# Optimization experiments

Measured on AMD Instinct MI355X. Metric: run time of the kernel, lower is better.

The kernel has to match this reference:

```python
import jax, jax.numpy as jnp
import numpy as np

N_NODES = 100000
N_EDGES = 1600000
NEG_SLOPE = 0.2  # DGL GATConv default leaky_relu slope
BN_EPS = 1e-5


def setup_inputs() -> dict:
    key = jax.random.key(0)
    ks = jax.random.split(key, 10)
    feats = jax.random.normal(ks[0], (N_NODES, 128), dtype=jnp.float32)
    src = jax.random.randint(ks[1], (N_EDGES,), 0, N_NODES, dtype=jnp.int64)
    dst = jax.random.randint(ks[2], (N_EDGES,), 0, N_NODES, dtype=jnp.int64)
    fc_w = jax.random.normal(ks[3], (256, 128), dtype=jnp.float32) * 0.05   # H*D x in_feats
    attn_l = jax.random.normal(ks[4], (4, 64), dtype=jnp.float32) * 0.05
    attn_r = jax.random.normal(ks[5], (4, 64), dtype=jnp.float32) * 0.05
    res_w = jax.random.normal(ks[6], (256, 128), dtype=jnp.float32) * 0.05  # residual projection
    bias = jax.random.normal(ks[7], (4, 64), dtype=jnp.float32) * 0.05
    gamma = jnp.ones((64,), dtype=jnp.float32)
    beta = jnp.zeros((64,), dtype=jnp.float32)
    return {"feats": feats, "src": src, "dst": dst, "fc_w": fc_w,
            "attn_l": attn_l, "attn_r": attn_r, "res_w": res_w,
            "bias": bias, "gamma": gamma, "beta": beta}


def reference(feats, src, dst, fc_w, attn_l, attn_r, res_w, bias, gamma, beta):
    N = feats.shape[0]
    H, D = attn_l.shape
    # projected features [N, H, D] (feat_drop is identity in eval mode)
    h = (feats @ fc_w.T).reshape(N, H, D)
    # per-node attention logits [N, H]
    el = jnp.sum(h * attn_l[None], axis=-1)
    er = jnp.sum(h * attn_r[None], axis=-1)
    # edge logits, leaky relu
    e = el[src] + er[dst]                       # [E, H]
    e = jnp.where(e > 0, e, NEG_SLOPE * e)
    # numerically stable segment softmax over incoming edges of each dst node
    m = jax.ops.segment_max(e, dst, num_segments=N)       # [N, H]
    ex = jnp.exp(e - m[dst])                               # [E, H]
    s = jax.ops.segment_sum(ex, dst, num_segments=N)       # [N, H]
    alpha = ex / s[dst]                                    # [E, H]
    # weighted message aggregation: scatter-add alpha * h_src into dst
    msg = h[src] * alpha[:, :, None]                       # [E, H, D]
    rst = jax.ops.segment_sum(msg, dst, num_segments=N)    # [N, H, D]
    # residual projection + bias + activation (elu)
    res = (feats @ res_w.T).reshape(N, H, D)
    rst = jax.nn.elu(rst + res + bias[None])
    # mean over heads -> [N, D]
    out = rst.mean(axis=1)
    # BatchNorm1d (training stats: biased variance over the node/batch axis)
    mu = out.mean(axis=0)
    var = out.var(axis=0)
    return (out - mu) * jax.lax.rsqrt(var + BN_EPS) * gamma + beta
```

## Files before the change

kernel.cpp:

```cpp
#include <hip/hip_runtime.h>

#define N_NODES 100000
#define N_EDGES 1600000
#define NEG_SLOPE 0.2f
#define BN_EPS 1e-5f

typedef __attribute__((ext_vector_type(8))) short short8;
typedef __attribute__((ext_vector_type(4))) float floatx4;
typedef __attribute__((ext_vector_type(8))) unsigned short u16x8;

static const size_t OFF_AB   = 0;
static const size_t OFF_BB   = 25624576;
static const size_t OFF_H    = 25755648;
static const size_t OFF_RES  = 76956672;
static const size_t OFF_EL   = 128156672;
static const size_t OFF_ER   = 129757184;
static const size_t OFF_DEG  = 131357184;
static const size_t OFF_RS   = 131757184;
static const size_t OFF_BNP  = 132157568;
static const size_t OFF_ESRC = 132557568;
static const size_t OFF_BS   = 142157568;

__device__ __forceinline__ unsigned short f2bf(float x) {
  unsigned int u = __float_as_uint(x);
  unsigned int r = (u + 0x7fffu + ((u >> 16) & 1u)) >> 16;
  return (unsigned short)r;
}
__device__ __forceinline__ float bf2f(unsigned short u) {
  return __uint_as_float(((unsigned int)u) << 16);
}

__global__ __launch_bounds__(256) void k_pre(
    const float* __restrict__ feats, const float* __restrict__ fc_w,
    const float* __restrict__ res_w, const int* __restrict__ dst,
    unsigned short* __restrict__ Ab, unsigned short* __restrict__ Bb,
    int* __restrict__ deg, unsigned short* __restrict__ hbuf,
    float* __restrict__ el, int* __restrict__ rank)
{
  const int b = blockIdx.x;
  if (b < 6256) {
    int c = b * 256 + threadIdx.x;
    int r = c >> 4, j = c & 15;
    unsigned short v[8];
    if (r < N_NODES) {
      const float* p = feats + (size_t)r * 128 + j * 8;
      float4 a = *(const float4*)p, bb = *(const float4*)(p + 4);
      v[0]=f2bf(a.x); v[1]=f2bf(a.y); v[2]=f2bf(a.z); v[3]=f2bf(a.w);
      v[4]=f2bf(bb.x); v[5]=f2bf(bb.y); v[6]=f2bf(bb.z); v[7]=f2bf(bb.w);
    } else {
      for (int i = 0; i < 8; i++) v[i] = 0;
    }
    size_t idx = (size_t)(r >> 7) * 2048 + ((r >> 4) & 7) * 256 + (j >> 2) * 64
               + (r & 15) + 16 * (j & 3);
    *(short8*)(Ab + idx * 8) = *(short8*)v;
  } else if (b < 12506) {
    int e = (b - 6256) * 256 + threadIdx.x;
    if (e < N_EDGES) rank[e] = atomicAdd(&deg[dst[e]], 1);
  } else if (b < 12538) {
    int c = (b - 12506) * 256 + threadIdx.x;
    int n = c >> 4, j = c & 15;
    const float* W = (n < 256) ? (fc_w + (size_t)n * 128) : (res_w + (size_t)(n - 256) * 128);
    const float* p = W + j * 8;
    float4 a = *(const float4*)p, bb = *(const float4*)(p + 4);
    unsigned short v[8];
    v[0]=f2bf(a.x); v[1]=f2bf(a.y); v[2]=f2bf(a.z); v[3]=f2bf(a.w);
    v[4]=f2bf(bb.x); v[5]=f2bf(bb.y); v[6]=f2bf(bb.z); v[7]=f2bf(bb.w);
    size_t idx = (size_t)(n >> 7) * 2048 + ((n >> 4) & 7) * 256 + (j >> 2) * 64
               + (n & 15) + 16 * (j & 3);
    *(short8*)(Bb + idx * 8) = *(short8*)v;
  } else {
    const int t = threadIdx.x;
    hbuf[(size_t)N_NODES * 256 + t] = 0;
    if (t < 4) el[N_NODES * 4 + t] = -1e30f;
  }
}

__global__ __launch_bounds__(256) void k_scan1(const int* __restrict__ deg,
                                               int* __restrict__ rs, int* __restrict__ bsums)
{
  __shared__ int tmp[256];
  const int t = threadIdx.x;
  const int base = blockIdx.x * 1024 + t * 4;
  int v0 = 0, v1 = 0, v2 = 0, v3 = 0;
  if (base + 0 < N_NODES) v0 = (deg[base + 0] + 3) & ~3;
  if (base + 1 < N_NODES) v1 = (deg[base + 1] + 3) & ~3;
  if (base + 2 < N_NODES) v2 = (deg[base + 2] + 3) & ~3;
  if (base + 3 < N_NODES) v3 = (deg[base + 3] + 3) & ~3;
  const int tsum = v0 + v1 + v2 + v3;
  tmp[t] = tsum;
  __syncthreads();
  for (int o = 1; o < 256; o <<= 1) {
    int x = (t >= o) ? tmp[t - o] : 0;
    __syncthreads();
    tmp[t] += x;
    __syncthreads();
  }
  const int excl = tmp[t] - tsum;
  if (base + 0 < N_NODES) rs[base + 0] = excl;
  if (base + 1 < N_NODES) rs[base + 1] = excl + v0;
  if (base + 2 < N_NODES) rs[base + 2] = excl + v0 + v1;
  if (base + 3 < N_NODES) rs[base + 3] = excl + v0 + v1 + v2;
  if (t == 255) bsums[blockIdx.x] = tmp[t];
}

__global__ __launch_bounds__(256) void k_scan3(int* __restrict__ rs,
                                               const int* __restrict__ bsums,
                                               const int* __restrict__ deg,
                                               int* __restrict__ esrc)
{
  __shared__ int sb[128];
  const int t = threadIdx.x;
  int raw = 0;
  if (t < 128) { raw = (t < 98) ? bsums[t] : 0; sb[t] = raw; }
  __syncthreads();
  for (int o = 1; o < 128; o <<= 1) {
    int x = (t >= o && t < 128) ? sb[t - o] : 0;
    __syncthreads();
    if (t < 128) sb[t] += x;
    __syncthreads();
  }
  if (t < 128) sb[t] -= raw;
  __syncthreads();
  const int i = blockIdx.x * 256 + t;
  if (i < N_NODES) {
    int v = rs[i] + sb[i >> 10];
    rs[i] = v;
    const int d = deg[i];
    const int pd = (d + 3) & ~3;
    for (int j = d; j < pd; j++) esrc[v + j] = N_NODES;
    if (i == N_NODES - 1) rs[N_NODES] = v + pd;
  }
}

__global__ __launch_bounds__(256) void k_place(const int* __restrict__ src,
                                               const int* __restrict__ dst,
                                               const int* __restrict__ rs,
                                               const int* __restrict__ rank,
                                               int* __restrict__ esrc)
{
  int e = blockIdx.x * 256 + threadIdx.x;
  if (e >= N_EDGES) return;
  esrc[rs[dst[e]] + rank[e]] = src[e];
}

__global__ __launch_bounds__(256) void k_mm(
    const unsigned short* __restrict__ Ab, const unsigned short* __restrict__ Bb,
    const float* __restrict__ bias, const float* __restrict__ attn_l,
    const float* __restrict__ attn_r,
    unsigned short* __restrict__ hbuf, unsigned short* __restrict__ resbuf,
    float* __restrict__ el, float* __restrict__ er)
{
  __shared__ unsigned short sA[16384];
  const int tid = threadIdx.x;
  const int w = tid >> 6, L = tid & 63;
  const int blk = blockIdx.x;

  {
    const unsigned short* ga = Ab + (size_t)blk * 16384;
    #pragma unroll
    for (int i = 0; i < 8; i++) {
      int off = (i * 256 + w * 64) * 8;
      __builtin_amdgcn_global_load_lds(
          (const __attribute__((address_space(1))) unsigned int*)(ga + off + L * 8),
          (__attribute__((address_space(3))) unsigned int*)(sA + off),
          16, 0, 0);
    }
  }
  const int mh = w & 1, nh = w >> 1;
  __syncthreads();

  for (int wb = 0; wb < 2; ++wb) {
    const int nb = blockIdx.y + wb * 2;
    floatx4 acc[4][4] = {};
    const unsigned short* gb = Bb + ((size_t)nb * 2048 + nh * 4 * 256) * 8 + L * 8;
    #pragma unroll
    for (int s = 0; s < 4; s++) {
      short8 a[4], b[4];
      #pragma unroll
      for (int t = 0; t < 4; t++)
        a[t] = *(const short8*)(sA + ((mh * 4 + t) * 256 + s * 64 + L) * 8);
      #pragma unroll
      for (int t = 0; t < 4; t++)
        b[t] = *(const short8*)(gb + ((size_t)t * 256 + s * 64) * 8);
      #pragma unroll
      for (int mt = 0; mt < 4; mt++)
        #pragma unroll
        for (int nt = 0; nt < 4; nt++)
          acc[mt][nt] = __builtin_amdgcn_mfma_f32_16x16x32_bf16(a[mt], b[nt], acc[mt][nt], 0, 0, 0);
    }

    const int q = L >> 4, cn = L & 15;
    const int r0 = blk * 128 + mh * 64;
    if (nb < 2) {
      const int head = nb * 2 + nh;
      const int col0 = nb * 128 + nh * 64;
      float al[4], ar[4];
      #pragma unroll
      for (int nt = 0; nt < 4; nt++) {
        al[nt] = attn_l[head * 64 + nt * 16 + cn];
        ar[nt] = attn_r[head * 64 + nt * 16 + cn];
      }
      #pragma unroll
      for (int mt = 0; mt < 4; mt++)
        #pragma unroll
        for (int r = 0; r < 4; r++) {
          const int row = r0 + mt * 16 + q * 4 + r;
          float pl = 0.f, pr = 0.f;
          #pragma unroll
          for (int nt = 0; nt < 4; nt++) {
            pl = fmaf(acc[mt][nt][r], al[nt], pl);
            pr = fmaf(acc[mt][nt][r], ar[nt], pr);
          }
          #pragma unroll
          for (int o = 1; o < 16; o <<= 1) {
            pl += __shfl_xor(pl, o, 64);
            pr += __shfl_xor(pr, o, 64);
          }
          if (row < N_NODES) {
            #pragma unroll
            for (int nt = 0; nt < 4; nt++)
              hbuf[(size_t)row * 256 + col0 + nt * 16 + cn] = f2bf(acc[mt][nt][r]);
            if (cn == 0) {
              el[row * 4 + head] = pl;
              er[row * 4 + head] = pr;
            }
          }
        }
    } else {
      const int rc0 = (nb - 2) * 128 + nh * 64;
      #pragma unroll
      for (int mt = 0; mt < 4; mt++)
        #pragma unroll
        for (int r = 0; r < 4; r++) {
          const int row = r0 + mt * 16 + q * 4 + r;
          if (row < N_NODES)
            #pragma unroll
            for (int nt = 0; nt < 4; nt++) {
              float v = acc[mt][nt][r] + bias[rc0 + nt * 16 + cn];
              resbuf[(size_t)row * 256 + rc0 + nt * 16 + cn] = f2bf(v);
            }
        }
    }
  }
}

#define RFL(x) __builtin_amdgcn_readfirstlane(x)

#define GATHER(X) do { \
  const int s_ = (lane & 32) ? sn##X.y : sn##X.x; \
  hv##X = *(const u16x8*)(hbuf + (size_t)s_ * 256 + li8); \
  ev##X = el[s_ * 4 + head]; \
} while (0)

#define PRO(X, B) do { \
  if ((B) < p_end) { sn##X = *(const int2*)(esrc + (B)); GATHER(X); } \
} while (0)

#define COMPUTE(X) do { \
  float e_ = ev##X + ern; \
  e_ = fmaxf(e_, NEG_SLOPE * e_); \
  const float w_ = __expf(e_); \
  ssum += w_; \
  accA.x = fmaf(w_, bf2f(hv##X[0]), accA.x); \
  accA.y = fmaf(w_, bf2f(hv##X[1]), accA.y); \
  accA.z = fmaf(w_, bf2f(hv##X[2]), accA.z); \
  accA.w = fmaf(w_, bf2f(hv##X[3]), accA.w); \
  accB.x = fmaf(w_, bf2f(hv##X[4]), accB.x); \
  accB.y = fmaf(w_, bf2f(hv##X[5]), accB.y); \
  accB.z = fmaf(w_, bf2f(hv##X[6]), accB.z); \
  accB.w = fmaf(w_, bf2f(hv##X[7]), accB.w); \
} while (0)

#define FIN(ND) do { \
  float st_ = ssum + __shfl_xor(ssum, 32, 64); \
  float a0_ = accA.x + __shfl_xor(accA.x, 32, 64); \
  float a1_ = accA.y + __shfl_xor(accA.y, 32, 64); \
  float a2_ = accA.z + __shfl_xor(accA.z, 32, 64); \
  float a3_ = accA.w + __shfl_xor(accA.w, 32, 64); \
  float a4_ = accB.x + __shfl_xor(accB.x, 32, 64); \
  float a5_ = accB.y + __shfl_xor(accB.y, 32, 64); \
  float a6_ = accB.z + __shfl_xor(accB.z, 32, 64); \
  float a7_ = accB.w + __shfl_xor(accB.w, 32, 64); \
  const float inv_ = (st_ > 0.f) ? (1.0f / st_) : 0.f; \
  a0_ = fmaf(a0_, inv_, bf2f(rv_cur[0])); \
  a1_ = fmaf(a1_, inv_, bf2f(rv_cur[1])); \
  a2_ = fmaf(a2_, inv_, bf2f(rv_cur[2])); \
  a3_ = fmaf(a3_, inv_, bf2f(rv_cur[3])); \
  a4_ = fmaf(a4_, inv_, bf2f(rv_cur[4])); \
  a5_ = fmaf(a5_, inv_, bf2f(rv_cur[5])); \
  a6_ = fmaf(a6_, inv_, bf2f(rv_cur[6])); \
  a7_ = fmaf(a7_, inv_, bf2f(rv_cur[7])); \
  a0_ = (a0_ > 0.f) ? a0_ : (__expf(a0_) - 1.f); \
  a1_ = (a1_ > 0.f) ? a1_ : (__expf(a1_) - 1.f); \
  a2_ = (a2_ > 0.f) ? a2_ : (__expf(a2_) - 1.f); \
  a3_ = (a3_ > 0.f) ? a3_ : (__expf(a3_) - 1.f); \
  a4_ = (a4_ > 0.f) ? a4_ : (__expf(a4_) - 1.f); \
  a5_ = (a5_ > 0.f) ? a5_ : (__expf(a5_) - 1.f); \
  a6_ = (a6_ > 0.f) ? a6_ : (__expf(a6_) - 1.f); \
  a7_ = (a7_ > 0.f) ? a7_ : (__expf(a7_) - 1.f); \
  a0_ += __shfl_xor(a0_, 8, 64);  a0_ += __shfl_xor(a0_, 16, 64); \
  a1_ += __shfl_xor(a1_, 8, 64);  a1_ += __shfl_xor(a1_, 16, 64); \
  a2_ += __shfl_xor(a2_, 8, 64);  a2_ += __shfl_xor(a2_, 16, 64); \
  a3_ += __shfl_xor(a3_, 8, 64);  a3_ += __shfl_xor(a3_, 16, 64); \
  a4_ += __shfl_xor(a4_, 8, 64);  a4_ += __shfl_xor(a4_, 16, 64); \
  a5_ += __shfl_xor(a5_, 8, 64);  a5_ += __shfl_xor(a5_, 16, 64); \
  a6_ += __shfl_xor(a6_, 8, 64);  a6_ += __shfl_xor(a6_, 16, 64); \
  a7_ += __shfl_xor(a7_, 8, 64);  a7_ += __shfl_xor(a7_, 16, 64); \
  if (lane < 8) { \
    float4 o1_, o2_; \
    o1_.x = a0_ * 0.25f; o1_.y = a1_ * 0.25f; o1_.z = a2_ * 0.25f; o1_.w = a3_ * 0.25f; \
    o2_.x = a4_ * 0.25f; o2_.y = a5_ * 0.25f; o2_.z = a6_ * 0.25f; o2_.w = a7_ * 0.25f; \
    *(float4*)(out + (size_t)(ND) * 64 + li8) = o1_; \
    *(float4*)(out + (size_t)(ND) * 64 + li8 + 4) = o2_; \
    atomicAdd(&ls[li8 + 0], o1_.x); atomicAdd(&ls[li8 + 1], o1_.y); \
    atomicAdd(&ls[li8 + 2], o1_.z); atomicAdd(&ls[li8 + 3], o1_.w); \
    atomicAdd(&ls[li8 + 4], o2_.x); atomicAdd(&ls[li8 + 5], o2_.y); \
    atomicAdd(&ls[li8 + 6], o2_.z); atomicAdd(&ls[li8 + 7], o2_.w); \
    atomicAdd(&lq[li8 + 0], o1_.x * o1_.x); atomicAdd(&lq[li8 + 1], o1_.y * o1_.y); \
    atomicAdd(&lq[li8 + 2], o1_.z * o1_.z); atomicAdd(&lq[li8 + 3], o1_.w * o1_.w); \
    atomicAdd(&lq[li8 + 4], o2_.x * o2_.x); atomicAdd(&lq[li8 + 5], o2_.y * o2_.y); \
    atomicAdd(&lq[li8 + 6], o2_.z * o2_.z); atomicAdd(&lq[li8 + 7], o2_.w * o2_.w); \
  } \
} while (0)

#define BOUNDARY() \
  while (p == nend) { \
    FIN(nu); \
    accA.x=0.f; accA.y=0.f; accA.z=0.f; accA.w=0.f; \
    accB.x=0.f; accB.y=0.f; accB.z=0.f; accB.w=0.f; ssum = 0.f; \
    nu++; \
    nend = nendN; ern = ernN; rv_cur = rvN; \
    const int f1_ = (nu + 1 < N_NODES) ? (nu + 1) : (N_NODES - 1); \
    const int f2_ = (nu + 2 <= N_NODES) ? (nu + 2) : N_NODES; \
    nendN = RFL(rs[f2_]); \
    ernN = er[f1_ * 4 + head]; \
    rvN = *(const u16x8*)(resbuf + (size_t)f1_ * 256 + li8); \
  }

#define STEP(CUR, GAT) do { \
  if (p + 12 < p_end) GATHER(GAT); \
  if (p + 16 < p_end) sn##CUR = *(const int2*)(esrc + p + 16); \
  __builtin_amdgcn_sched_barrier(0); \
  BOUNDARY(); \
  COMPUTE(CUR); \
} while (0)

__global__ __launch_bounds__(256, 4) void k_agg(
    const unsigned short* __restrict__ hbuf, const unsigned short* __restrict__ resbuf,
    const float* __restrict__ el, const float* __restrict__ er,
    const int* __restrict__ rs, const int* __restrict__ esrc,
    float* __restrict__ out, float* __restrict__ bn)
{
  __shared__ float ls[64], lq[64];
  const int lane = threadIdx.x & 63;
  const int li = lane & 31;
  const int head = li >> 3;
  const int li8 = li * 8;
  const int wid = blockIdx.x * 4 + (threadIdx.x >> 6);
  const int nW = gridDim.x * 4;

  if (threadIdx.x < 64) { ls[threadIdx.x] = 0.f; lq[threadIdx.x] = 0.f; }
  __syncthreads();

  const int n0 = (int)(((long long)wid * N_NODES) / nW);
  const int n1 = (int)(((long long)(wid + 1) * N_NODES) / nW);

  if (n0 < n1) {
    int nu = RFL(n0);
    const int p_end = RFL(rs[n1]);
    int nend = RFL(rs[nu + 1]);
    int f1 = (nu + 1 < N_NODES) ? (nu + 1) : (N_NODES - 1);
    int f2 = (nu + 2 <= N_NODES) ? (nu + 2) : N_NODES;
    int nendN = RFL(rs[f2]);
    float ern  = er[nu * 4 + head];
    float ernN = er[f1 * 4 + head];
    u16x8 rv_cur = *(const u16x8*)(resbuf + (size_t)nu * 256 + li8);
    u16x8 rvN    = *(const u16x8*)(resbuf + (size_t)f1 * 256 + li8);

    float4 accA = make_float4(0.f, 0.f, 0.f, 0.f);
    float4 accB = make_float4(0.f, 0.f, 0.f, 0.f);
    float ssum = 0.f;

    int2 snA, snB, snC, snD, snE, snF, snG, snH;
    float evA, evB, evC, evD, evE, evF, evG, evH;
    u16x8 hvA, hvB, hvC, hvD, hvE, hvF, hvG, hvH;

    int p = RFL(rs[nu]);
    PRO(A, p);      PRO(B, p + 2);  PRO(C, p + 4);  PRO(D, p + 6);
    PRO(E, p + 8);  PRO(F, p + 10);
    if (p + 12 < p_end) snG = *(const int2*)(esrc + p + 12);
    if (p + 14 < p_end) snH = *(const int2*)(esrc + p + 14);
    __builtin_amdgcn_sched_barrier(0);

    while (p < p_end) {
      STEP(A, G); p += 2; if (p >= p_end) break;
      STEP(B, H); p += 2; if (p >= p_end) break;
      STEP(C, A); p += 2; if (p >= p_end) break;
      STEP(D, B); p += 2; if (p >= p_end) break;
      STEP(E, C); p += 2; if (p >= p_end) break;
      STEP(F, D); p += 2; if (p >= p_end) break;
      STEP(G, E); p += 2; if (p >= p_end) break;
      STEP(H, F); p += 2;
    }

    while (nu < n1) {
      FIN(nu);
      accA.x=0.f; accA.y=0.f; accA.z=0.f; accA.w=0.f;
      accB.x=0.f; accB.y=0.f; accB.z=0.f; accB.w=0.f; ssum = 0.f;
      nu++;
      if (nu < n1) rv_cur = *(const u16x8*)(resbuf + (size_t)nu * 256 + li8);
    }
  }

  __syncthreads();
  const int t = threadIdx.x;
  if (t < 64)       atomicAdd(&bn[t * 16], ls[t]);
  else if (t < 128) atomicAdd(&bn[t * 16], lq[t - 64]);
}

__global__ __launch_bounds__(256) void k_bn_apply(float* __restrict__ out,
                                                  const float* __restrict__ bn,
                                                  const float* __restrict__ gamma,
                                                  const float* __restrict__ beta)
{
  __shared__ float sc[64], sh[64];
  const int t = threadIdx.x;
  if (t < 64) {
    float mean = bn[t * 16] * (1.0f / N_NODES);
    float var = bn[(t + 64) * 16] * (1.0f / N_NODES) - mean * mean;
    float s = gamma[t] * rsqrtf(var + BN_EPS);
    sc[t] = s;
    sh[t] = beta[t] - mean * s;
  }
  __syncthreads();
  const int i = blockIdx.x * 256 + t;
  if (i >= N_NODES * 16) return;
  const int d0 = (i & 15) * 4;
  float4 v = *(float4*)(out + (size_t)i * 4);
  v.x = fmaf(v.x, sc[d0 + 0], sh[d0 + 0]);
  v.y = fmaf(v.y, sc[d0 + 1], sh[d0 + 1]);
  v.z = fmaf(v.z, sc[d0 + 2], sh[d0 + 2]);
  v.w = fmaf(v.w, sc[d0 + 3], sh[d0 + 3]);
  *(float4*)(out + (size_t)i * 4) = v;
}

extern "C" void kernel_launch(void* const* d_in, const int* in_sizes, int n_in,
                              void* d_out, int out_size, void* d_ws, size_t ws_size,
                              hipStream_t stream)
{
  const float* feats  = (const float*)d_in[0];
  const int*   src    = (const int*)d_in[1];
  const int*   dst    = (const int*)d_in[2];
  const float* fc_w   = (const float*)d_in[3];
  const float* attn_l = (const float*)d_in[4];
  const float* attn_r = (const float*)d_in[5];
  const float* res_w  = (const float*)d_in[6];
  const float* bias   = (const float*)d_in[7];
  const float* gamma  = (const float*)d_in[8];
  const float* beta   = (const float*)d_in[9];

  char* ws = (char*)d_ws;
  unsigned short* Ab     = (unsigned short*)(ws + OFF_AB);
  unsigned short* Bb     = (unsigned short*)(ws + OFF_BB);
  unsigned short* hbuf   = (unsigned short*)(ws + OFF_H);
  unsigned short* resbuf = (unsigned short*)(ws + OFF_RES);
  float* elb    = (float*)(ws + OFF_EL);
  float* erb    = (float*)(ws + OFF_ER);
  int*   deg    = (int*)(ws + OFF_DEG);
  int*   rsb    = (int*)(ws + OFF_RS);
  float* bnb    = (float*)(ws + OFF_BNP);
  int*   esrc   = (int*)(ws + OFF_ESRC);
  int*   bsums  = (int*)(ws + OFF_BS);
  float* outp   = (float*)d_out;
  int*   rankp  = (int*)d_out;

  hipMemsetAsync(deg, 0, N_NODES * sizeof(int), stream);
  hipMemsetAsync(bnb, 0, 128 * 16 * sizeof(float), stream);

  k_pre<<<12539, 256, 0, stream>>>(feats, fc_w, res_w, dst, Ab, Bb, deg, hbuf, elb, rankp);
  k_scan1<<<98, 256, 0, stream>>>(deg, rsb, bsums);
  k_scan3<<<391, 256, 0, stream>>>(rsb, bsums, deg, esrc);
  k_place<<<6250, 256, 0, stream>>>(src, dst, rsb, rankp, esrc);
  k_mm<<<dim3(782, 2), 256, 0, stream>>>(Ab, Bb, bias, attn_l, attn_r,
                                         hbuf, resbuf, elb, erb);
  k_agg<<<2048, 256, 0, stream>>>(hbuf, resbuf, elb, erb, rsb, esrc, outp, bnb);
  k_bn_apply<<<6250, 256, 0, stream>>>(outp, bnb, gamma, beta);
}
```

Baseline: 454.6 us.

## Precompute per-edge exp attention weights during CSR placement, drop bound checks in aggregation

Moves k_place after the matmul and has it compute each edge's leaky-relu and exp logit for all four heads, storing them as bf16 in CSR order in a buffer that reuses the Ab region. The aggregation kernel then loads one precomputed weight per edge instead of randomly gathering el[src] and computing exp. Padding slots and a 16-entry tail are zero-filled so the prefetch loop can drop its bounds checks. The trade is an extra scattered write of 8 bytes per edge, plus bf16 rounding of the attention weights, which may cost accuracy.

```diff
diff --git a/kernel.cpp b/kernel.cpp
--- a/kernel.cpp
+++ b/kernel.cpp
@@ -35,7 +35,7 @@
     const float* __restrict__ res_w, const int* __restrict__ dst,
     unsigned short* __restrict__ Ab, unsigned short* __restrict__ Bb,
     int* __restrict__ deg, unsigned short* __restrict__ hbuf,
-    float* __restrict__ el, int* __restrict__ rank)
+    int* __restrict__ rank)
 {
   const int b = blockIdx.x;
   if (b < 6256) {
@@ -69,9 +69,7 @@
                + (n & 15) + 16 * (j & 3);
     *(short8*)(Bb + idx * 8) = *(short8*)v;
   } else {
-    const int t = threadIdx.x;
-    hbuf[(size_t)N_NODES * 256 + t] = 0;
-    if (t < 4) el[N_NODES * 4 + t] = -1e30f;
+    hbuf[(size_t)N_NODES * 256 + threadIdx.x] = 0;
   }
 }
 
@@ -128,19 +126,11 @@
     const int d = deg[i];
     const int pd = (d + 3) & ~3;
     for (int j = d; j < pd; j++) esrc[v + j] = N_NODES;
-    if (i == N_NODES - 1) rs[N_NODES] = v + pd;
-  }
-}
-
-__global__ __launch_bounds__(256) void k_place(const int* __restrict__ src,
-                                               const int* __restrict__ dst,
-                                               const int* __restrict__ rs,
-                                               const int* __restrict__ rank,
-                                               int* __restrict__ esrc)
-{
-  int e = blockIdx.x * 256 + threadIdx.x;
-  if (e >= N_EDGES) return;
-  esrc[rs[dst[e]] + rank[e]] = src[e];
+    if (i == N_NODES - 1) {
+      rs[N_NODES] = v + pd;
+      for (int j = 0; j < 16; j++) esrc[v + pd + j] = N_NODES;
+    }
+  }
 }
 
 __global__ __launch_bounds__(256) void k_mm(
@@ -244,31 +234,60 @@
   }
 }
 
+__global__ __launch_bounds__(256) void k_place(
+    const int* __restrict__ src, const int* __restrict__ dst,
+    const int* __restrict__ rs, const int* __restrict__ rank,
+    const int* __restrict__ deg,
+    const float* __restrict__ el, const float* __restrict__ er,
+    int* __restrict__ esrc, unsigned short* __restrict__ wb)
+{
+  const int b = blockIdx.x;
+  if (b < 6250) {
+    const int e = b * 256 + threadIdx.x;
+    if (e >= N_EDGES) return;
+    const int d = dst[e], s = src[e];
+    const int pos = rs[d] + rank[e];
+    esrc[pos] = s;
+    const float4 l4 = *(const float4*)(el + (size_t)s * 4);
+    const float4 r4 = *(const float4*)(er + (size_t)d * 4);
+    float e0 = l4.x + r4.x; e0 = fmaxf(e0, NEG_SLOPE * e0);
+    float e1 = l4.y + r4.y; e1 = fmaxf(e1, NEG_SLOPE * e1);
+    float e2 = l4.z + r4.z; e2 = fmaxf(e2, NEG_SLOPE * e2);
+    float e3 = l4.w + r4.w; e3 = fmaxf(e3, NEG_SLOPE * e3);
+    ushort4 w4;
+    w4.x = f2bf(__expf(e0)); w4.y = f2bf(__expf(e1));
+    w4.z = f2bf(__expf(e2)); w4.w = f2bf(__expf(e3));
+    *(ushort4*)(wb + (size_t)pos * 4) = w4;
+  } else {
+    const int i = (b - 6250) * 256 + threadIdx.x;
+    if (i >= N_NODES) return;
+    const int d = deg[i], pd = (d + 3) & ~3;
+    const int v = rs[i];
+    const ushort4 z4 = make_ushort4(0, 0, 0, 0);
+    for (int j = d; j < pd; j++) *(ushort4*)(wb + (size_t)(v + j) * 4) = z4;
+    if (i == N_NODES - 1)
+      for (int j = 0; j < 16; j++) *(ushort4*)(wb + (size_t)(v + pd + j) * 4) = z4;
+  }
+}
+
 #define RFL(x) __builtin_amdgcn_readfirstlane(x)
 
-#define GATHER(X) do { \
+#define GATHER(X, BB) do { \
   const int s_ = (lane & 32) ? sn##X.y : sn##X.x; \
   hv##X = *(const u16x8*)(hbuf + (size_t)s_ * 256 + li8); \
-  ev##X = el[s_ * 4 + head]; \
+  wv##X = bf2f(wb[(size_t)((BB) + half) * 4 + head]); \
 } while (0)
 
-#define PRO(X, B) do { \
-  if ((B) < p_end) { sn##X = *(const int2*)(esrc + (B)); GATHER(X); } \
-} while (0)
-
 #define COMPUTE(X) do { \
-  float e_ = ev##X + ern; \
-  e_ = fmaxf(e_, NEG_SLOPE * e_); \
-  const float w_ = __expf(e_); \
-  ssum += w_; \
-  accA.x = fmaf(w_, bf2f(hv##X[0]), accA.x); \
-  accA.y = fmaf(w_, bf2f(hv##X[1]), accA.y); \
-  accA.z = fmaf(w_, bf2f(hv##X[2]), accA.z); \
-  accA.w = fmaf(w_, bf2f(hv##X[3]), accA.w); \
-  accB.x = fmaf(w_, bf2f(hv##X[4]), accB.x); \
-  accB.y = fmaf(w_, bf2f(hv##X[5]), accB.y); \
-  accB.z = fmaf(w_, bf2f(hv##X[6]), accB.z); \
-  accB.w = fmaf(w_, bf2f(hv##X[7]), accB.w); \
+  ssum += wv##X; \
+  accA.x = fmaf(wv##X, bf2f(hv##X[0]), accA.x); \
+  accA.y = fmaf(wv##X, bf2f(hv##X[1]), accA.y); \
+  accA.z = fmaf(wv##X, bf2f(hv##X[2]), accA.z); \
+  accA.w = fmaf(wv##X, bf2f(hv##X[3]), accA.w); \
+  accB.x = fmaf(wv##X, bf2f(hv##X[4]), accB.x); \
+  accB.y = fmaf(wv##X, bf2f(hv##X[5]), accB.y); \
+  accB.z = fmaf(wv##X, bf2f(hv##X[6]), accB.z); \
+  accB.w = fmaf(wv##X, bf2f(hv##X[7]), accB.w); \
 } while (0)
 
 #define FIN(ND) do { \
@@ -329,17 +348,16 @@
     accA.x=0.f; accA.y=0.f; accA.z=0.f; accA.w=0.f; \
     accB.x=0.f; accB.y=0.f; accB.z=0.f; accB.w=0.f; ssum = 0.f; \
     nu++; \
-    nend = nendN; ern = ernN; rv_cur = rvN; \
+    nend = nendN; rv_cur = rvN; \
     const int f1_ = (nu + 1 < N_NODES) ? (nu + 1) : (N_NODES - 1); \
     const int f2_ = (nu + 2 <= N_NODES) ? (nu + 2) : N_NODES; \
     nendN = RFL(rs[f2_]); \
-    ernN = er[f1_ * 4 + head]; \
     rvN = *(const u16x8*)(resbuf + (size_t)f1_ * 256 + li8); \
   }
 
 #define STEP(CUR, GAT) do { \
-  if (p + 12 < p_end) GATHER(GAT); \
-  if (p + 16 < p_end) sn##CUR = *(const int2*)(esrc + p + 16); \
+  GATHER(GAT, p + 12); \
+  sn##CUR = *(const int2*)(esrc + p + 16); \
   __builtin_amdgcn_sched_barrier(0); \
   BOUNDARY(); \
   COMPUTE(CUR); \
@@ -347,13 +365,14 @@
 
 __global__ __launch_bounds__(256, 4) void k_agg(
     const unsigned short* __restrict__ hbuf, const unsigned short* __restrict__ resbuf,
-    const float* __restrict__ el, const float* __restrict__ er,
+    const unsigned short* __restrict__ wb,
     const int* __restrict__ rs, const int* __restrict__ esrc,
     float* __restrict__ out, float* __restrict__ bn)
 {
   __shared__ float ls[64], lq[64];
   const int lane = threadIdx.x & 63;
   const int li = lane & 31;
+  const int half = lane >> 5;
   const int head = li >> 3;
   const int li8 = li * 8;
   const int wid = blockIdx.x * 4 + (threadIdx.x >> 6);
@@ -372,8 +391,6 @@
     int f1 = (nu + 1 < N_NODES) ? (nu + 1) : (N_NODES - 1);
     int f2 = (nu + 2 <= N_NODES) ? (nu + 2) : N_NODES;
     int nendN = RFL(rs[f2]);
-    float ern  = er[nu * 4 + head];
-    float ernN = er[f1 * 4 + head];
     u16x8 rv_cur = *(const u16x8*)(resbuf + (size_t)nu * 256 + li8);
     u16x8 rvN    = *(const u16x8*)(resbuf + (size_t)f1 * 256 + li8);
 
@@ -382,14 +399,18 @@
     float ssum = 0.f;
 
     int2 snA, snB, snC, snD, snE, snF, snG, snH;
-    float evA, evB, evC, evD, evE, evF, evG, evH;
+    float wvA, wvB, wvC, wvD, wvE, wvF, wvG, wvH;
     u16x8 hvA, hvB, hvC, hvD, hvE, hvF, hvG, hvH;
 
     int p = RFL(rs[nu]);
-    PRO(A, p);      PRO(B, p + 2);  PRO(C, p + 4);  PRO(D, p + 6);
-    PRO(E, p + 8);  PRO(F, p + 10);
-    if (p + 12 < p_end) snG = *(const int2*)(esrc + p + 12);
-    if (p + 14 < p_end) snH = *(const int2*)(esrc + p + 14);
+    snA = *(const int2*)(esrc + p);      GATHER(A, p);
+    snB = *(const int2*)(esrc + p + 2);  GATHER(B, p + 2);
+    snC = *(const int2*)(esrc + p + 4);  GATHER(C, p + 4);
+    snD = *(const int2*)(esrc + p + 6);  GATHER(D, p + 6);
+    snE = *(const int2*)(esrc + p + 8);  GATHER(E, p + 8);
+    snF = *(const int2*)(esrc + p + 10); GATHER(F, p + 10);
+    snG = *(const int2*)(esrc + p + 12);
+    snH = *(const int2*)(esrc + p + 14);
     __builtin_amdgcn_sched_barrier(0);
 
     while (p < p_end) {
@@ -461,6 +482,7 @@
 
   char* ws = (char*)d_ws;
   unsigned short* Ab     = (unsigned short*)(ws + OFF_AB);
+  unsigned short* wbuf   = (unsigned short*)(ws + OFF_AB);
   unsigned short* Bb     = (unsigned short*)(ws + OFF_BB);
   unsigned short* hbuf   = (unsigned short*)(ws + OFF_H);
   unsigned short* resbuf = (unsigned short*)(ws + OFF_RES);
@@ -477,12 +499,12 @@
   hipMemsetAsync(deg, 0, N_NODES * sizeof(int), stream);
   hipMemsetAsync(bnb, 0, 128 * 16 * sizeof(float), stream);
 
-  k_pre<<<12539, 256, 0, stream>>>(feats, fc_w, res_w, dst, Ab, Bb, deg, hbuf, elb, rankp);
+  k_pre<<<12539, 256, 0, stream>>>(feats, fc_w, res_w, dst, Ab, Bb, deg, hbuf, rankp);
   k_scan1<<<98, 256, 0, stream>>>(deg, rsb, bsums);
   k_scan3<<<391, 256, 0, stream>>>(rsb, bsums, deg, esrc);
-  k_place<<<6250, 256, 0, stream>>>(src, dst, rsb, rankp, esrc);
   k_mm<<<dim3(782, 2), 256, 0, stream>>>(Ab, Bb, bias, attn_l, attn_r,
                                          hbuf, resbuf, elb, erb);
-  k_agg<<<2048, 256, 0, stream>>>(hbuf, resbuf, elb, erb, rsb, esrc, outp, bnb);
+  k_place<<<6641, 256, 0, stream>>>(src, dst, rsb, rankp, deg, elb, erb, esrc, wbuf);
+  k_agg<<<2048, 256, 0, stream>>>(hbuf, resbuf, wbuf, rsb, esrc, outp, bnb);
   k_bn_apply<<<6250, 256, 0, stream>>>(outp, bnb, gamma, beta);
 }
```

New measurement: 849.4 us. 86.9% more time.
